# Performance work log

Measured on AMD Instinct MI355X. Metric: run time of the kernel, lower is better.

## Reference

```python
import jax, jax.numpy as jnp
import numpy as np
import math
from jax import lax

B, E, NC, NT, H, W, NH = 16, 256, 8, 8, 64, 64, 8
Q = NC * (NT // 2 + 1)   # 40 prototype tokens
HW = H * W               # in_feature = 4096
OF = 64                  # out_feature; OF*OF == HW required by broadcast


def setup_inputs() -> dict:
    key = jax.random.key(0)
    ks = iter(jax.random.split(key, 48))
    n = lambda s, sc=0.02: jax.random.normal(next(ks), s, jnp.float32) * sc
    return dict(
        query_prototypes=jax.random.normal(next(ks), (B, Q, E), jnp.float32),
        image_embed=jax.random.normal(next(ks), (B, E, H, W), jnp.float32),
        mask_embed=jax.random.normal(next(ks), (B, NC, H, W), jnp.float32),
        masks=jax.random.uniform(next(ks), (B, NC, H, W), jnp.float32),
        ln_g=jnp.ones((E,), jnp.float32), ln_b=jnp.zeros((E,), jnp.float32),
        qw=n((E, E)), qb=jnp.zeros((E,), jnp.float32),
        xp1_w=n((E + NC, E)), xp1_b=jnp.zeros((E,), jnp.float32),
        xp2_w=n((E, E)), xp2_b=jnp.zeros((E,), jnp.float32),
        ln2_g=jnp.ones((E,), jnp.float32), ln2_b=jnp.zeros((E,), jnp.float32),
        dw_w=n((3, 3, 1, E)), dw_b=jnp.zeros((E,), jnp.float32),
        kw=n((E, E)), kb=jnp.zeros((E,), jnp.float32),
        vw=n((E, E)), vb=jnp.zeros((E,), jnp.float32),
        ic_w=n((E,)), ic_b=jnp.zeros((1,), jnp.float32),
        mc_w=n((NC,)), mc_b=jnp.zeros((1,), jnp.float32),
        ipw=n((HW, OF)), ipb=jnp.zeros((OF,), jnp.float32),
        mpw=n((HW, OF)), mpb=jnp.zeros((OF,), jnp.float32),
        cw=n((Q,), 0.1), cb=jnp.zeros((Q,), jnp.float32),
        alpha=jnp.full((HW,), 0.001, jnp.float32),
        beta=jnp.full((HW,), 0.001, jnp.float32),
        ow=n((E, E)), ob=jnp.zeros((E,), jnp.float32),
    )


def _ln(x, g, b, axis):
    m = jnp.mean(x, axis=axis, keepdims=True)
    v = jnp.var(x, axis=axis, keepdims=True)
    return (x - m) * lax.rsqrt(v + 1e-5) * g + b


def reference(query_prototypes, image_embed, mask_embed, masks, ln_g, ln_b, qw, qb,
              xp1_w, xp1_b, xp2_w, xp2_b, ln2_g, ln2_b, dw_w, dw_b, kw, kb, vw, vb,
              ic_w, ic_b, mc_w, mc_b, ipw, ipb, mpw, mpb, cw, cb, alpha, beta, ow, ob):
    hd = E // NH
    # q branch: LayerNorm + Linear
    q = _ln(query_prototypes, ln_g, ln_b, -1) @ qw + qb                      # [B,Q,E]
    # x branch: 1x1 conv + gelu -> 1x1 conv + channel-LN -> depthwise 3x3
    xcat = jnp.concatenate([image_embed, mask_embed], axis=1)                # [B,E+NC,H,W]
    x = jax.nn.gelu(jnp.einsum('bchw,cd->bdhw', xcat, xp1_w) + xp1_b[None, :, None, None], approximate=False)
    x = jnp.einsum('bchw,cd->bdhw', x, xp2_w) + xp2_b[None, :, None, None]
    x = _ln(x, ln2_g[None, :, None, None], ln2_b[None, :, None, None], 1)
    x = lax.conv_general_dilated(x, dw_w, (1, 1), 'SAME',
                                 dimension_numbers=('NCHW', 'HWIO', 'NCHW'),
                                 feature_group_count=E) + dw_b[None, :, None, None]
    x = x.reshape(B, E, HW).transpose(0, 2, 1)                               # [B,HW,E]
    k = (x @ kw + kb).reshape(B, HW, NH, hd).transpose(0, 2, 1, 3)           # [B,NH,HW,hd]
    v = (x @ vw + vb).reshape(B, HW, NH, hd).transpose(0, 2, 1, 3)
    qh = q.reshape(B, Q, NH, hd).transpose(0, 2, 1, 3)                       # [B,NH,Q,hd]
    # class-attention additive bias from rank-1 image x mask outer product
    att_image = (jnp.einsum('behw,e->bhw', image_embed, ic_w) + ic_b[0]).reshape(B, HW) @ ipw + ipb  # [B,OF]
    att_mask = (jnp.einsum('bchw,c->bhw', mask_embed, mc_w) + mc_b[0]).reshape(B, HW) @ mpw + mpb    # [B,OF]
    att_class = att_image[:, :, None] * att_mask[:, None, :]                 # [B,OF,OF]
    att_class = att_class[:, None, :, :] * cw[None, :, None, None] + cb[None, :, None, None]  # 1x1 conv 1->Q
    att_class = att_class.reshape(B, Q, HW)[:, None]                         # [B,1,Q,HW]
    # mask-modulated query-key scores
    att_q = jnp.einsum('bnqc,bnkc->bnqk', qh, k)                             # [B,NH,Q,HW]
    att_q = att_q.reshape(B, NH, NC, NT // 2 + 1, HW) * masks.reshape(B, 1, NC, 1, HW)
    att_q = att_q.reshape(B, NH, Q, HW)
    w = (att_class * alpha + att_q * beta) / math.sqrt(hd)
    w = jax.nn.softmax(w, axis=-1)
    out = jnp.einsum('bnqk,bnkc->bnqc', w, v)                                # [B,NH,Q,hd]
    out = out.transpose(0, 2, 1, 3).reshape(B, Q, E)
    return out @ ow + ob
```

## Files before the change

### kernel.cpp

```cpp
#include <hip/hip_runtime.h>
#include <math.h>

constexpr int B_ = 16, E_ = 256, NC_ = 8, Q_ = 40, H_ = 64, W_ = 64, HW_ = 4096;
constexpr int NH_ = 8, HD_ = 32, OF_ = 64;
constexpr int KP1_ = 320;
constexpr int NPART_ = 32;
constexpr int CH2_ = 32;
constexpr int KVS_ = 512;

typedef __attribute__((ext_vector_type(8))) unsigned short us8;
typedef __attribute__((ext_vector_type(8))) short s8b;
typedef __attribute__((ext_vector_type(4))) short s4b;
typedef __attribute__((ext_vector_type(4))) float f32x4;

__device__ __forceinline__ float gelu_f(float x) {
  return 0.5f * x * (1.0f + erff(x * 0.70710678118654752f));
}
__device__ __forceinline__ float bf2f(unsigned short u) {
  return __uint_as_float(((unsigned int)u) << 16);
}
__device__ __forceinline__ unsigned short f2bf(float f) {
  unsigned int u = __float_as_uint(f);
  u = u + 0x7fff + ((u >> 16) & 1);
  return (unsigned short)(u >> 16);
}
__device__ __forceinline__ unsigned int cvtpk_bf16(float a, float b) {
  unsigned int r;
  asm("v_cvt_pk_bf16_f32 %0, %1, %2" : "=v"(r) : "v"(a), "v"(b));
  return r;
}
__device__ __forceinline__ void gl_lds16(const unsigned short* g, unsigned short* l) {
  __builtin_amdgcn_global_load_lds(
      (const __attribute__((address_space(1))) unsigned int*)g,
      (__attribute__((address_space(3))) unsigned int*)l, 16, 0, 0);
}

__global__ __launch_bounds__(256)
void misc1(const float* __restrict__ w1, const float* __restrict__ w2,
           const float* __restrict__ wk, const float* __restrict__ wv,
           const float* __restrict__ kb, const float* __restrict__ vb,
           unsigned short* __restrict__ o1, unsigned short* __restrict__ o2,
           unsigned short* __restrict__ okv, float* __restrict__ kvbias,
           const float* __restrict__ img, const float* __restrict__ msk,
           unsigned short* __restrict__ xcatT,
           const float* __restrict__ qp, const float* __restrict__ ln_g,
           const float* __restrict__ ln_b, const float* __restrict__ qw,
           const float* __restrict__ qb, float* __restrict__ qbuf,
           const float* __restrict__ icw, const float* __restrict__ icb,
           const float* __restrict__ mcw, const float* __restrict__ mcb,
           float* __restrict__ timg, float* __restrict__ tmsk) {
  __shared__ __align__(16) float smem[64 * 65];
  const int bid = blockIdx.x;
  const int t = threadIdx.x;
  if (bid < 4 * KP1_) {
    const int which = bid / KP1_;
    const int k = bid % KP1_;
    const int n = t;
    if (which == 0) {
      float v = (k < 264) ? w1[(size_t)k * E_ + n] : 0.f;
      o1[(size_t)n * KP1_ + k] = f2bf(v);
    } else if (k < 256) {
      if (which == 1) {
        o2[(size_t)n * 256 + k] = f2bf(w2[(size_t)k * E_ + n]);
      } else if (which == 2) {
        okv[(size_t)n * 256 + k] = f2bf(wk[(size_t)k * E_ + n]);
        if (k == 0) kvbias[n] = kb[n];
      } else {
        okv[(size_t)(256 + n) * 256 + k] = f2bf(wv[(size_t)k * E_ + n]);
        if (k == 0) kvbias[256 + n] = vb[n];
      }
    }
  } else if (bid < 4 * KP1_ + 5120) {
    const int id = bid - 4 * KP1_;
    const int p0 = (id & 63) * 64;
    const int k0 = ((id >> 6) % 5) * 64;
    const int b = id / 320;
    float (*tile)[65] = (float(*)[65])smem;
    const int pg = t & 15;
    const int kg = t >> 4;
    f32x4 v4[4];
    #pragma unroll
    for (int ki = 0; ki < 4; ++ki) {
      const int k = k0 + kg * 4 + ki;
      if (k < 256)
        v4[ki] = *(const f32x4*)(img + ((size_t)b * E_ + k) * HW_ + p0 + pg * 4);
      else if (k < 264)
        v4[ki] = *(const f32x4*)(msk + ((size_t)b * NC_ + (k - 256)) * HW_ + p0 + pg * 4);
      else
        v4[ki] = (f32x4){0.f, 0.f, 0.f, 0.f};
    }
    #pragma unroll
    for (int ki = 0; ki < 4; ++ki)
      #pragma unroll
      for (int j = 0; j < 4; ++j)
        tile[pg * 4 + j][kg * 4 + ki] = v4[ki][j];
    __syncthreads();
    const int pr = t >> 2, ch = t & 3;
    unsigned short st[16];
    #pragma unroll
    for (int i = 0; i < 16; ++i) st[i] = f2bf(tile[pr][ch * 16 + i]);
    unsigned short* dst = xcatT + ((size_t)b * HW_ + p0 + pr) * KP1_ + k0 + ch * 16;
    *(us8*)dst = *(const us8*)&st[0];
    *(us8*)(dst + 8) = *(const us8*)&st[8];
  } else if (bid < 4 * KP1_ + 5120 + 640) {
    const int row = bid - (4 * KP1_ + 5120);
    float* xs = smem;
    float* rs = smem + 272;
    float* rs2 = smem + 280;
    float* sm = smem + 288;
    float x = qp[(size_t)row * E_ + t];
    float s = x, s2 = x * x;
    #pragma unroll
    for (int o = 32; o > 0; o >>= 1) { s += __shfl_down(s, o, 64); s2 += __shfl_down(s2, o, 64); }
    if ((t & 63) == 0) { rs[t >> 6] = s; rs2[t >> 6] = s2; }
    __syncthreads();
    if (t == 0) {
      float S = rs[0] + rs[1] + rs[2] + rs[3];
      float S2 = rs2[0] + rs2[1] + rs2[2] + rs2[3];
      float m = S * (1.0f / E_);
      sm[0] = m;
      sm[1] = rsqrtf(S2 * (1.0f / E_) - m * m + 1e-5f);
    }
    __syncthreads();
    x = (x - sm[0]) * sm[1] * ln_g[t] + ln_b[t];
    xs[t] = x;
    __syncthreads();
    float acc = qb[t];
    #pragma unroll 8
    for (int c = 0; c < E_; ++c) acc += xs[c] * qw[(size_t)c * E_ + t];
    qbuf[(size_t)row * E_ + t] = acc;
  } else {
    const int id = bid - (4 * KP1_ + 5120 + 640);
    const int b = id >> 4;
    const int chunk = id & 15;
    const int lane = t & 63, seg = t >> 6;
    const int p = chunk * 256 + lane * 4;
    f32x4 (*red)[64] = (f32x4(*)[64])smem;
    f32x4 s = (f32x4){0.f, 0.f, 0.f, 0.f};
    const float* ib = img + (size_t)b * E_ * HW_ + p;
    #pragma unroll 8
    for (int e = seg * 64; e < seg * 64 + 64; ++e) {
      const f32x4 v = *(const f32x4*)(ib + (size_t)e * HW_);
      s += v * icw[e];
    }
    red[seg][lane] = s;
    __syncthreads();
    if (seg == 0) {
      f32x4 tot = red[0][lane] + red[1][lane] + red[2][lane] + red[3][lane];
      #pragma unroll
      for (int j = 0; j < 4; ++j) tot[j] += icb[0];
      *(f32x4*)(timg + (size_t)b * HW_ + p) = tot;
      f32x4 s2;
      #pragma unroll
      for (int j = 0; j < 4; ++j) s2[j] = mcb[0];
      const float* mb = msk + (size_t)b * NC_ * HW_ + p;
      #pragma unroll
      for (int c = 0; c < NC_; ++c) {
        const f32x4 mv = *(const f32x4*)(mb + (size_t)c * HW_);
        s2 += mv * mcw[c];
      }
      *(f32x4*)(tmsk + (size_t)b * HW_ + p) = s2;
    }
  }
}

template<int EPI, int KP, int OSTR, int NN>
__global__ __launch_bounds__(256, 4)
void hgemm(const unsigned short* __restrict__ A, const unsigned short* __restrict__ Wt,
           const float* __restrict__ bias, unsigned short* __restrict__ out) {
  constexpr int NT = KP / 64;
  __shared__ __align__(16) unsigned short As[128 * 64];
  __shared__ __align__(16) unsigned short Bs[64 * 64];
  const int t = threadIdx.x;
  const int bid = blockIdx.x;
  const int xcd = bid & 7;
  const int grp = bid >> 3;
  const int m0 = ((grp / NN) * 8 + xcd) * 128;
  const int n0 = (grp % NN) * 64;
  const int w = t >> 6, lane = t & 63;
  const int c = lane & 15, g = lane >> 4;
  const int wm = (w & 1) * 64, wn = (w >> 1) * 32;

  f32x4 acc[4][2];
  #pragma unroll
  for (int i = 0; i < 4; ++i)
    #pragma unroll
    for (int j = 0; j < 2; ++j) acc[i][j] = (f32x4){0.f, 0.f, 0.f, 0.f};

  for (int kt = 0; kt < NT; ++kt) {
    if (kt) __syncthreads();
    #pragma unroll
    for (int i = 0; i < 4; ++i) {
      const int f = i * 256 + t;
      const int row = f >> 3, s = f & 7;
      gl_lds16(A + (size_t)(m0 + row) * KP + kt * 64 + (s ^ (row & 7)) * 8, As + f * 8);
    }
    #pragma unroll
    for (int i = 0; i < 2; ++i) {
      const int f = i * 256 + t;
      const int row = f >> 3, s = f & 7;
      gl_lds16(Wt + (size_t)(n0 + row) * KP + kt * 64 + (s ^ (row & 7)) * 8, Bs + f * 8);
    }
    __syncthreads();
    #pragma unroll
    for (int ks = 0; ks < 2; ++ks) {
      s8b af[4], bf[2];
      #pragma unroll
      for (int mf = 0; mf < 4; ++mf) {
        const int row = wm + mf * 16 + c;
        af[mf] = *(const s8b*)&As[row * 64 + ((ks * 4 + g) ^ (row & 7)) * 8];
      }
      #pragma unroll
      for (int nf = 0; nf < 2; ++nf) {
        const int row = wn + nf * 16 + c;
        bf[nf] = *(const s8b*)&Bs[row * 64 + ((ks * 4 + g) ^ (row & 7)) * 8];
      }
      #pragma unroll
      for (int mf = 0; mf < 4; ++mf)
        #pragma unroll
        for (int nf = 0; nf < 2; ++nf)
          acc[mf][nf] = __builtin_amdgcn_mfma_f32_16x16x32_bf16(af[mf], bf[nf], acc[mf][nf], 0, 0, 0);
    }
  }

  float bv[2];
  #pragma unroll
  for (int nf = 0; nf < 2; ++nf) bv[nf] = bias[n0 + wn + nf * 16 + c];
  __syncthreads();
  #pragma unroll
  for (int mf = 0; mf < 4; ++mf)
    #pragma unroll
    for (int r = 0; r < 4; ++r) {
      const int row = wm + mf * 16 + g * 4 + r;
      #pragma unroll
      for (int nf = 0; nf < 2; ++nf) {
        float v = acc[mf][nf][r] + bv[nf];
        if constexpr (EPI == 0) v = gelu_f(v);
        As[row * 64 + wn + nf * 16 + c] = f2bf(v);
      }
    }
  __syncthreads();
  #pragma unroll
  for (int i = 0; i < 4; ++i) {
    const int f = i * 256 + t;
    const int row = f >> 3, sl = f & 7;
    *(us8*)(out + (size_t)(m0 + row) * OSTR + n0 + sl * 8) = *(const us8*)&As[row * 64 + sl * 8];
  }
}

__global__ __launch_bounds__(256)
void rowstats(const unsigned short* __restrict__ X, float* __restrict__ mean,
              float* __restrict__ rstd) {
  const int row = blockIdx.x * 4 + (threadIdx.x >> 6);
  const int lane = threadIdx.x & 63;
  const uint2 u = *(const uint2*)(X + (size_t)row * E_ + lane * 4);
  float a = bf2f(u.x & 0xffff), b = bf2f(u.x >> 16);
  float c = bf2f(u.y & 0xffff), d = bf2f(u.y >> 16);
  float s = a + b + c + d;
  float s2 = a * a + b * b + c * c + d * d;
  #pragma unroll
  for (int o = 32; o > 0; o >>= 1) { s += __shfl_down(s, o, 64); s2 += __shfl_down(s2, o, 64); }
  if (lane == 0) {
    const float m = s * (1.0f / E_);
    mean[row] = m;
    rstd[row] = rsqrtf(s2 * (1.0f / E_) - m * m + 1e-5f);
  }
}

__global__ __launch_bounds__(256)
void attvec_p(const float* __restrict__ timg, const float* __restrict__ tmsk,
              const float* __restrict__ ipw, const float* __restrict__ mpw,
              float* __restrict__ part) {
  const int chunk = blockIdx.x;
  const int b = blockIdx.y;
  const int mat = blockIdx.z;
  const int o = threadIdx.x & 63, ps = threadIdx.x >> 6;
  const float* tv = (mat ? tmsk : timg) + (size_t)b * HW_ + chunk * 256;
  const float* wp = (mat ? mpw : ipw) + (size_t)chunk * 256 * OF_;
  float s = 0.f;
  #pragma unroll 8
  for (int i = 0; i < 64; ++i) {
    const int p = ps * 64 + i;
    s += tv[p] * wp[(size_t)p * OF_ + o];
  }
  __shared__ float red[4][64];
  red[ps][o] = s;
  __syncthreads();
  if (ps == 0)
    part[(((size_t)b * 2 + mat) * 16 + chunk) * OF_ + o] =
        red[0][o] + red[1][o] + red[2][o] + red[3][o];
}

__global__ __launch_bounds__(256)
void attbias2(const float* __restrict__ part, const float* __restrict__ ipb,
              const float* __restrict__ mpb, const float* __restrict__ alpha,
              const float* __restrict__ beta, float* __restrict__ A1,
              float* __restrict__ asd, float* __restrict__ bsd) {
  __shared__ float aiL[64], amL[64];
  const int b = blockIdx.x;
  const int t = threadIdx.x;
  if (t < 128) {
    const int mat = t >> 6, o = t & 63;
    float v = (mat ? mpb : ipb)[o];
    #pragma unroll
    for (int c = 0; c < 16; ++c)
      v += part[(((size_t)b * 2 + mat) * 16 + c) * OF_ + o];
    if (mat) amL[o] = v; else aiL[o] = v;
  }
  __syncthreads();
  const float scl = 0.17677669529663687f;
  #pragma unroll
  for (int it = 0; it < 16; ++it) {
    const int p = it * 256 + t;
    A1[(size_t)b * HW_ + p] = aiL[p >> 6] * amL[p & 63] * alpha[p] * scl;
    if (b == 0) {
      asd[p] = alpha[p] * scl;
      bsd[p] = beta[p] * scl;
    }
  }
}

__global__ __launch_bounds__(256, 4)
void dwconv_ln4(const unsigned short* __restrict__ X2, const float* __restrict__ mean,
                const float* __restrict__ rstd, const float* __restrict__ g2,
                const float* __restrict__ b2, const float* __restrict__ wgt,
                const float* __restrict__ cbias, unsigned short* __restrict__ out) {
  __shared__ __align__(16) unsigned short xsh[108 * 128];
  __shared__ float msh[108], rsh[108];
  const int t = threadIdx.x;
  const int w0 = blockIdx.x * 16;
  const int h0 = blockIdx.y * 4;
  const int b = blockIdx.z >> 1;
  const int dh = blockIdx.z & 1;
  const int dl = t & 127;
  const int cg = t >> 7;
  const int dgl = dh * 128 + dl;
  const size_t bbase = (size_t)b * HW_;
  for (int f = t; f < 108 * 16; f += 256) {
    const int pix = f >> 4, sl = f & 15;
    const int s = pix / 18, i = pix % 18;
    const int hh = h0 - 1 + s, ww = w0 - 1 + i;
    const bool ok = (hh >= 0 && hh < H_ && ww >= 0 && ww < W_);
    const size_t p = ok ? (bbase + hh * W_ + ww) : bbase;
    gl_lds16(X2 + p * E_ + dh * 128 + sl * 8, &xsh[f * 8]);
  }
  if (t < 108) {
    const int pix = t;
    const int s = pix / 18, i = pix % 18;
    const int hh = h0 - 1 + s, ww = w0 - 1 + i;
    if (hh >= 0 && hh < H_ && ww >= 0 && ww < W_) {
      const size_t p = bbase + hh * W_ + ww;
      msh[pix] = mean[p];
      rsh[pix] = rstd[p];
    } else {
      msh[pix] = 0.f;
      rsh[pix] = 0.f;
    }
  }
  float wq[9];
  #pragma unroll
  for (int i = 0; i < 9; ++i) wq[i] = wgt[i * E_ + dgl];
  const float gg = g2[dgl], bb = b2[dgl], bias = cbias[dgl];
  __syncthreads();
  float o[4][8];
  #pragma unroll
  for (int oy = 0; oy < 4; ++oy)
    #pragma unroll
    for (int j = 0; j < 8; ++j) o[oy][j] = bias;
  #pragma unroll
  for (int s = 0; s < 6; ++s) {
    const int hh = h0 - 1 + s;
    if (hh < 0 || hh >= H_) continue;
    float r[10];
    #pragma unroll
    for (int i = 0; i < 10; ++i) {
      const int rc = cg * 8 + i;
      const int ww = w0 - 1 + rc;
      if (ww >= 0 && ww < W_) {
        const int pix = s * 18 + rc;
        const float x = bf2f(xsh[pix * 128 + dl]);
        r[i] = (x - msh[pix]) * rsh[pix] * gg + bb;
      } else r[i] = 0.f;
    }
    #pragma unroll
    for (int ky = 0; ky < 3; ++ky) {
      const int oy = s - ky;
      if (oy < 0 || oy >= 4) continue;
      const float w_0 = wq[ky * 3], w_1 = wq[ky * 3 + 1], w_2 = wq[ky * 3 + 2];
      #pragma unroll
      for (int j = 0; j < 8; ++j)
        o[oy][j] += r[j] * w_0 + r[j + 1] * w_1 + r[j + 2] * w_2;
    }
  }
  #pragma unroll
  for (int oy = 0; oy < 4; ++oy) {
    const size_t ob_ = bbase + (h0 + oy) * W_ + w0 + cg * 8;
    #pragma unroll
    for (int j = 0; j < 8; ++j) out[(ob_ + j) * E_ + dgl] = f2bf(o[oy][j]);
  }
}

#if __has_builtin(__builtin_amdgcn_mfma_f32_16x16x16bf16_1k)
#define HAVE_MFMA16 1
#else
#define HAVE_MFMA16 0
#endif

__global__ __launch_bounds__(64)
void attn_mfma1w(const float* __restrict__ qbuf, const unsigned short* __restrict__ kv,
                 const float* __restrict__ masks,
                 const float* __restrict__ A1, const float* __restrict__ asd,
                 const float* __restrict__ bsd, const float* __restrict__ cw,
                 const float* __restrict__ cb,
                 float* __restrict__ pacc, float* __restrict__ pm, float* __restrict__ pl) {
  const int bid = blockIdx.x;
  const int xcd = bid & 7;
  const int n = (bid >> 3) & 7;
  const int pb = ((bid >> 6) << 3) | xcd;
  const int ch = pb & 31;
  const int b = pb >> 5;
  const int lane = threadIdx.x;
  const int c = lane & 15, g = lane >> 4;
  __shared__ __align__(16) unsigned short Vt[32 * 72];
#if !HAVE_MFMA16
  __shared__ __align__(16) unsigned short Pl[48 * 72];
#endif

  const size_t bhw = (size_t)b * HW_;
  const int koff = n * HD_;
  const int voff = 256 + koff;
  const int pbase = ch * 128;

  s8b kf2[2][4];
  #pragma unroll
  for (int tile = 0; tile < 2; ++tile) {
    const int p0 = pbase + tile * 64;
    #pragma unroll
    for (int mt = 0; mt < 4; ++mt)
      kf2[tile][mt] = *(const s8b*)(kv + (bhw + p0 + mt * 16 + c) * KVS_ + koff + g * 8);
  }

  s8b qf[3];
  float cwq[3], cbq[3];
  int cls[3];
  #pragma unroll
  for (int nt = 0; nt < 3; ++nt) {
    const int q = nt * 16 + c;
    unsigned short tmp[8];
    if (q < Q_) {
      const float* qp = qbuf + ((size_t)b * Q_ + q) * E_ + koff + g * 8;
      const float4 f0 = *(const float4*)qp;
      const float4 f1 = *(const float4*)(qp + 4);
      tmp[0] = f2bf(f0.x); tmp[1] = f2bf(f0.y); tmp[2] = f2bf(f0.z); tmp[3] = f2bf(f0.w);
      tmp[4] = f2bf(f1.x); tmp[5] = f2bf(f1.y); tmp[6] = f2bf(f1.z); tmp[7] = f2bf(f1.w);
      cwq[nt] = cw[q]; cbq[nt] = cb[q];
    } else {
      #pragma unroll
      for (int i = 0; i < 8; ++i) tmp[i] = 0;
      cwq[nt] = 0.f; cbq[nt] = 0.f;
    }
    qf[nt] = *(const s8b*)tmp;
    cls[nt] = min(q / 5, NC_ - 1);
  }

  f32x4 acc_oT[3][2];
  #pragma unroll
  for (int qt = 0; qt < 3; ++qt)
    #pragma unroll
    for (int dt = 0; dt < 2; ++dt) acc_oT[qt][dt] = (f32x4){0.f, 0.f, 0.f, 0.f};
  float m_r[3] = {-1e30f, -1e30f, -1e30f};
  float l_r[3] = {0.f, 0.f, 0.f};
  float scv[3] = {1.f, 1.f, 1.f};

  #pragma unroll
  for (int tile = 0; tile < 2; ++tile) {
    const int p0 = pbase + tile * 64;
    us8 vr[4];
    #pragma unroll
    for (int cp = 0; cp < 4; ++cp)
      vr[cp] = *(const us8*)(kv + (bhw + p0 + lane) * KVS_ + voff + cp * 8);
    f32x4 sa[3][4];
    __builtin_amdgcn_s_setprio(1);
    #pragma unroll
    for (int nt = 0; nt < 3; ++nt)
      #pragma unroll
      for (int mt = 0; mt < 4; ++mt)
        sa[nt][mt] = __builtin_amdgcn_mfma_f32_16x16x32_bf16(kf2[tile][mt], qf[nt],
                     (f32x4){0.f, 0.f, 0.f, 0.f}, 0, 0, 0);
    __builtin_amdgcn_s_setprio(0);
    #pragma unroll
    for (int cp = 0; cp < 4; ++cp) {
      #pragma unroll
      for (int i = 0; i < 8; ++i) Vt[(cp * 8 + i) * 72 + lane] = vr[cp][i];
    }
    f32x4 A1v[4], asv[4], bsv[4];
    #pragma unroll
    for (int mt = 0; mt < 4; ++mt) {
      const int pp = p0 + mt * 16 + g * 4;
      A1v[mt] = *(const f32x4*)(A1 + bhw + pp);
      asv[mt] = *(const f32x4*)(asd + pp);
      bsv[mt] = *(const f32x4*)(bsd + pp);
    }
    uint2 pwv[3][4];
    #pragma unroll
    for (int nt = 0; nt < 3; ++nt) {
      const float* mrow = masks + ((size_t)b * NC_ + cls[nt]) * HW_;
      f32x4 att[4];
      #pragma unroll
      for (int mt = 0; mt < 4; ++mt) {
        const f32x4 mk = *(const f32x4*)(mrow + p0 + mt * 16 + g * 4);
        att[mt] = A1v[mt] * cwq[nt] + asv[mt] * cbq[nt] + sa[nt][mt] * mk * bsv[mt];
      }
      float mx = -1e30f;
      #pragma unroll
      for (int mt = 0; mt < 4; ++mt)
        mx = fmaxf(mx, fmaxf(fmaxf(att[mt][0], att[mt][1]), fmaxf(att[mt][2], att[mt][3])));
      mx = fmaxf(mx, __shfl_xor(mx, 16));
      mx = fmaxf(mx, __shfl_xor(mx, 32));
      const float newm = fmaxf(m_r[nt], mx);
      const float sc = __expf(m_r[nt] - newm);
      m_r[nt] = newm;
      scv[nt] = sc;
      float sum = 0.f;
      #pragma unroll
      for (int mt = 0; mt < 4; ++mt) {
        #pragma unroll
        for (int i = 0; i < 4; ++i) att[mt][i] = __expf(att[mt][i] - newm);
        sum += (att[mt][0] + att[mt][1]) + (att[mt][2] + att[mt][3]);
        pwv[nt][mt].x = cvtpk_bf16(att[mt][0], att[mt][1]);
        pwv[nt][mt].y = cvtpk_bf16(att[mt][2], att[mt][3]);
      }
      sum += __shfl_xor(sum, 16);
      sum += __shfl_xor(sum, 32);
      l_r[nt] = l_r[nt] * sc + sum;
    }
    #pragma unroll
    for (int nt = 0; nt < 3; ++nt)
      #pragma unroll
      for (int dt = 0; dt < 2; ++dt)
        #pragma unroll
        for (int r = 0; r < 4; ++r) acc_oT[nt][dt][r] *= scv[nt];
#if HAVE_MFMA16
    __builtin_amdgcn_s_setprio(1);
    #pragma unroll
    for (int mt = 0; mt < 4; ++mt) {
      s4b vf[2];
      #pragma unroll
      for (int dt = 0; dt < 2; ++dt)
        vf[dt] = *(const s4b*)&Vt[(dt * 16 + c) * 72 + mt * 16 + g * 4];
      #pragma unroll
      for (int nt = 0; nt < 3; ++nt)
        #pragma unroll
        for (int dt = 0; dt < 2; ++dt)
          acc_oT[nt][dt] = __builtin_amdgcn_mfma_f32_16x16x16bf16_1k(
              vf[dt], *(const s4b*)&pwv[nt][mt], acc_oT[nt][dt], 0, 0, 0);
    }
    __builtin_amdgcn_s_setprio(0);
#else
    #pragma unroll
    for (int nt = 0; nt < 3; ++nt)
      #pragma unroll
      for (int mt = 0; mt < 4; ++mt)
        *(uint2*)&Pl[(nt * 16 + c) * 72 + mt * 16 + g * 4] = pwv[nt][mt];
    #pragma unroll
    for (int ks = 0; ks < 2; ++ks) {
      s8b pf[3], vf2[2];
      #pragma unroll
      for (int nt = 0; nt < 3; ++nt)
        pf[nt] = *(const s8b*)&Pl[(nt * 16 + c) * 72 + ks * 32 + g * 8];
      #pragma unroll
      for (int dt = 0; dt < 2; ++dt)
        vf2[dt] = *(const s8b*)&Vt[(dt * 16 + c) * 72 + ks * 32 + g * 8];
      #pragma unroll
      for (int nt = 0; nt < 3; ++nt)
        #pragma unroll
        for (int dt = 0; dt < 2; ++dt)
          acc_oT[nt][dt] = __builtin_amdgcn_mfma_f32_16x16x32_bf16(vf2[dt], pf[nt], acc_oT[nt][dt], 0, 0, 0);
    }
#endif
  }
  const int pidx = ((b * NH_ + n) * NPART_) + ch;
  #pragma unroll
  for (int nt = 0; nt < 3; ++nt) {
    const int q = nt * 16 + c;
    if (q < Q_) {
      #pragma unroll
      for (int dt = 0; dt < 2; ++dt)
        *(f32x4*)&pacc[((size_t)pidx * Q_ + q) * HD_ + dt * 16 + g * 4] = acc_oT[nt][dt];
    }
  }
  if (g == 0) {
    #pragma unroll
    for (int nt = 0; nt < 3; ++nt) {
      const int q = nt * 16 + c;
      if (q < Q_) {
        pm[(size_t)pidx * Q_ + q] = m_r[nt];
        pl[(size_t)pidx * Q_ + q] = l_r[nt];
      }
    }
  }
}

__global__ __launch_bounds__(256)
void cfinal(const float* __restrict__ pacc, const float* __restrict__ pm,
            const float* __restrict__ pl, const float* __restrict__ ow,
            const float* __restrict__ ob, float* __restrict__ out) {
  __shared__ float xs[E_];
  const int row = blockIdx.x;
  const int q = row % Q_;
  const int b = row / Q_;
  const int e = threadIdx.x;
  const int n = e >> 5, d = e & 31;
  const int base = (b * NH_ + n) * NPART_;
  float M = -1e30f;
  #pragma unroll
  for (int cc = 0; cc < NPART_; ++cc) M = fmaxf(M, pm[(size_t)(base + cc) * Q_ + q]);
  float L = 0.f, O = 0.f;
  #pragma unroll
  for (int cc = 0; cc < NPART_; ++cc) {
    const size_t o2 = (size_t)(base + cc) * Q_ + q;
    const float w = __expf(pm[o2] - M);
    L += pl[o2] * w;
    O += pacc[o2 * HD_ + d] * w;
  }
  xs[e] = O / L;
  __syncthreads();
  float acc = ob[e];
  #pragma unroll 8
  for (int c = 0; c < E_; ++c) acc += xs[c] * ow[(size_t)c * E_ + e];
  out[(size_t)row * E_ + e] = acc;
}

extern "C" void kernel_launch(void* const* d_in, const int* in_sizes, int n_in,
                              void* d_out, int out_size, void* d_ws, size_t ws_size,
                              hipStream_t stream) {
  (void)in_sizes; (void)n_in; (void)out_size; (void)ws_size;
  const float* qp    = (const float*)d_in[0];
  const float* img   = (const float*)d_in[1];
  const float* msk   = (const float*)d_in[2];
  const float* masks = (const float*)d_in[3];
  const float* ln_g  = (const float*)d_in[4];
  const float* ln_b  = (const float*)d_in[5];
  const float* qw    = (const float*)d_in[6];
  const float* qb    = (const float*)d_in[7];
  const float* x1w   = (const float*)d_in[8];
  const float* x1b   = (const float*)d_in[9];
  const float* x2w   = (const float*)d_in[10];
  const float* x2b   = (const float*)d_in[11];
  const float* ln2g  = (const float*)d_in[12];
  const float* ln2b  = (const float*)d_in[13];
  const float* dww   = (const float*)d_in[14];
  const float* dwb   = (const float*)d_in[15];
  const float* kw    = (const float*)d_in[16];
  const float* kb    = (const float*)d_in[17];
  const float* vw    = (const float*)d_in[18];
  const float* vb    = (const float*)d_in[19];
  const float* icw   = (const float*)d_in[20];
  const float* icb   = (const float*)d_in[21];
  const float* mcw   = (const float*)d_in[22];
  const float* mcb   = (const float*)d_in[23];
  const float* ipw   = (const float*)d_in[24];
  const float* ipb   = (const float*)d_in[25];
  const float* mpw   = (const float*)d_in[26];
  const float* mpb   = (const float*)d_in[27];
  const float* cw    = (const float*)d_in[28];
  const float* cb    = (const float*)d_in[29];
  const float* alpha = (const float*)d_in[30];
  const float* beta  = (const float*)d_in[31];
  const float* ow    = (const float*)d_in[32];
  const float* ob    = (const float*)d_in[33];

  char* wsb = (char*)d_ws;
  const size_t MB = 1024 * 1024;
  unsigned short* xcatT = (unsigned short*)(wsb);
  unsigned short* xf    = xcatT;
  unsigned short* x1buf = (unsigned short*)(wsb + 42 * MB);
  unsigned short* x2    = (unsigned short*)(wsb + 76 * MB);
  unsigned short* kv    = (unsigned short*)(wsb + 76 * MB);
  unsigned short* wt1 = (unsigned short*)(wsb + 141 * MB);
  unsigned short* wt2 = wt1 + 256 * KP1_;
  unsigned short* wtkv = wt2 + 256 * 256;
  float* fb    = (float*)(wsb + 143 * MB);
  float* kvbias = fb;
  float* qbuf  = kvbias + 512;
  float* meanb = qbuf + (size_t)B_ * Q_ * E_;
  float* rstdb = meanb + (size_t)B_ * HW_;
  float* timg  = rstdb + (size_t)B_ * HW_;
  float* tmsk  = timg + (size_t)B_ * HW_;
  float* A1b   = tmsk + (size_t)B_ * HW_;
  float* asdb  = A1b + (size_t)B_ * HW_;
  float* bsdb  = asdb + HW_;
  float* pacc  = bsdb + HW_;
  float* pmb   = pacc + (size_t)B_ * NH_ * NPART_ * Q_ * HD_;
  float* plb   = pmb + (size_t)B_ * NH_ * NPART_ * Q_;
  float* partv = plb + (size_t)B_ * NH_ * NPART_ * Q_;

  misc1<<<dim3(4 * KP1_ + 5120 + 640 + 256), dim3(256), 0, stream>>>(
      x1w, x2w, kw, vw, kb, vb, wt1, wt2, wtkv, kvbias,
      img, msk, xcatT, qp, ln_g, ln_b, qw, qb, qbuf,
      icw, icb, mcw, mcb, timg, tmsk);
  attvec_p<<<dim3(16, B_, 2), dim3(256), 0, stream>>>(timg, tmsk, ipw, mpw, partv);
  attbias2<<<dim3(B_), dim3(256), 0, stream>>>(partv, ipb, mpb, alpha, beta, A1b, asdb, bsdb);
  hgemm<0, KP1_, 256, 4><<<dim3(512 * 4), dim3(256), 0, stream>>>(xcatT, wt1, x1b, x1buf);
  hgemm<1, 256, 256, 4><<<dim3(512 * 4), dim3(256), 0, stream>>>(x1buf, wt2, x2b, x2);
  rowstats<<<dim3(B_ * HW_ / 4), dim3(256), 0, stream>>>(x2, meanb, rstdb);
  dwconv_ln4<<<dim3(4, 16, B_ * 2), dim3(256), 0, stream>>>(x2, meanb, rstdb, ln2g, ln2b, dww, dwb, xf);
  hgemm<1, 256, KVS_, 8><<<dim3(512 * 8), dim3(256), 0, stream>>>(xf, wtkv, kvbias, kv);
  attn_mfma1w<<<dim3(CH2_ * NH_ * B_), dim3(64), 0, stream>>>(qbuf, kv, masks, A1b, asdb, bsdb,
                                                              cw, cb, pacc, pmb, plb);
  cfinal<<<dim3(B_ * Q_), dim3(256), 0, stream>>>(pacc, pmb, plb, ow, ob, (float*)d_out);
}
```

Baseline: 202.1 us.

## Fuse input transpose and bf16 conversion into first GEMM's A-tile load

Removes the separate transpose pass that wrote a bf16 pixel-major copy of image and mask embeddings, and instead has a new GEMM kernel load fp32 activations directly, convert with packed bf16 instructions and store swizzled into LDS. This eliminates a large intermediate write and re-read. The trade-off is that each N-tile block re-reads the fp32 input, doing more global traffic per tile and conversion work inside the GEMM loop, without the async global-to-LDS path for A.

```diff
diff --git a/kernel.cpp b/kernel.cpp
--- a/kernel.cpp
+++ b/kernel.cpp
@@ -42,7 +42,6 @@
            unsigned short* __restrict__ o1, unsigned short* __restrict__ o2,
            unsigned short* __restrict__ okv, float* __restrict__ kvbias,
            const float* __restrict__ img, const float* __restrict__ msk,
-           unsigned short* __restrict__ xcatT,
            const float* __restrict__ qp, const float* __restrict__ ln_g,
            const float* __restrict__ ln_b, const float* __restrict__ qw,
            const float* __restrict__ qb, float* __restrict__ qbuf,
@@ -70,40 +69,8 @@
         if (k == 0) kvbias[256 + n] = vb[n];
       }
     }
-  } else if (bid < 4 * KP1_ + 5120) {
-    const int id = bid - 4 * KP1_;
-    const int p0 = (id & 63) * 64;
-    const int k0 = ((id >> 6) % 5) * 64;
-    const int b = id / 320;
-    float (*tile)[65] = (float(*)[65])smem;
-    const int pg = t & 15;
-    const int kg = t >> 4;
-    f32x4 v4[4];
-    #pragma unroll
-    for (int ki = 0; ki < 4; ++ki) {
-      const int k = k0 + kg * 4 + ki;
-      if (k < 256)
-        v4[ki] = *(const f32x4*)(img + ((size_t)b * E_ + k) * HW_ + p0 + pg * 4);
-      else if (k < 264)
-        v4[ki] = *(const f32x4*)(msk + ((size_t)b * NC_ + (k - 256)) * HW_ + p0 + pg * 4);
-      else
-        v4[ki] = (f32x4){0.f, 0.f, 0.f, 0.f};
-    }
-    #pragma unroll
-    for (int ki = 0; ki < 4; ++ki)
-      #pragma unroll
-      for (int j = 0; j < 4; ++j)
-        tile[pg * 4 + j][kg * 4 + ki] = v4[ki][j];
-    __syncthreads();
-    const int pr = t >> 2, ch = t & 3;
-    unsigned short st[16];
-    #pragma unroll
-    for (int i = 0; i < 16; ++i) st[i] = f2bf(tile[pr][ch * 16 + i]);
-    unsigned short* dst = xcatT + ((size_t)b * HW_ + p0 + pr) * KP1_ + k0 + ch * 16;
-    *(us8*)dst = *(const us8*)&st[0];
-    *(us8*)(dst + 8) = *(const us8*)&st[8];
-  } else if (bid < 4 * KP1_ + 5120 + 640) {
-    const int row = bid - (4 * KP1_ + 5120);
+  } else if (bid < 4 * KP1_ + 640) {
+    const int row = bid - 4 * KP1_;
     float* xs = smem;
     float* rs = smem + 272;
     float* rs2 = smem + 280;
@@ -130,7 +97,7 @@
     for (int c = 0; c < E_; ++c) acc += xs[c] * qw[(size_t)c * E_ + t];
     qbuf[(size_t)row * E_ + t] = acc;
   } else {
-    const int id = bid - (4 * KP1_ + 5120 + 640);
+    const int id = bid - (4 * KP1_ + 640);
     const int b = id >> 4;
     const int chunk = id & 15;
     const int lane = t & 63, seg = t >> 6;
@@ -245,6 +212,110 @@
     const int f = i * 256 + t;
     const int row = f >> 3, sl = f & 7;
     *(us8*)(out + (size_t)(m0 + row) * OSTR + n0 + sl * 8) = *(const us8*)&As[row * 64 + sl * 8];
+  }
+}
+
+__global__ __launch_bounds__(256, 4)
+void hgemm1f(const float* __restrict__ img, const float* __restrict__ msk,
+             const unsigned short* __restrict__ Wt,
+             const float* __restrict__ bias, unsigned short* __restrict__ out) {
+  constexpr int KP = KP1_;
+  constexpr int NT = 5;
+  constexpr int NN = 4;
+  __shared__ __align__(16) unsigned short As[128 * 64];
+  __shared__ __align__(16) unsigned short Bs[64 * 64];
+  const int t = threadIdx.x;
+  const int bid = blockIdx.x;
+  const int xcd = bid & 7;
+  const int grp = bid >> 3;
+  const int m0 = ((grp / NN) * 8 + xcd) * 128;
+  const int n0 = (grp % NN) * 64;
+  const int b = m0 >> 12;
+  const int px0 = m0 & 4095;
+  const int w = t >> 6, lane = t & 63;
+  const int c = lane & 15, g = lane >> 4;
+  const int wm = (w & 1) * 64, wn = (w >> 1) * 32;
+  const int pg = t & 31;
+  const int kg = t >> 5;
+
+  f32x4 acc[4][2];
+  #pragma unroll
+  for (int i = 0; i < 4; ++i)
+    #pragma unroll
+    for (int j = 0; j < 2; ++j) acc[i][j] = (f32x4){0.f, 0.f, 0.f, 0.f};
+
+  for (int kt = 0; kt < NT; ++kt) {
+    if (kt) __syncthreads();
+    #pragma unroll
+    for (int i = 0; i < 2; ++i) {
+      const int f = i * 256 + t;
+      const int row = f >> 3, s = f & 7;
+      gl_lds16(Wt + (size_t)(n0 + row) * KP + kt * 64 + (s ^ (row & 7)) * 8, Bs + f * 8);
+    }
+    f32x4 ar[8];
+    #pragma unroll
+    for (int i = 0; i < 8; ++i) {
+      const int k = kt * 64 + kg * 8 + i;
+      if (k < 256)
+        ar[i] = *(const f32x4*)(img + ((size_t)b * E_ + k) * HW_ + px0 + pg * 4);
+      else if (k < 264)
+        ar[i] = *(const f32x4*)(msk + ((size_t)b * NC_ + (k - 256)) * HW_ + px0 + pg * 4);
+      else
+        ar[i] = (f32x4){0.f, 0.f, 0.f, 0.f};
+    }
+    #pragma unroll
+    for (int j = 0; j < 4; ++j) {
+      const int px = pg * 4 + j;
+      uint4 pk;
+      pk.x = cvtpk_bf16(ar[0][j], ar[1][j]);
+      pk.y = cvtpk_bf16(ar[2][j], ar[3][j]);
+      pk.z = cvtpk_bf16(ar[4][j], ar[5][j]);
+      pk.w = cvtpk_bf16(ar[6][j], ar[7][j]);
+      *(uint4*)&As[px * 64 + (kg ^ (px & 7)) * 8] = pk;
+    }
+    __syncthreads();
+    #pragma unroll
+    for (int ks = 0; ks < 2; ++ks) {
+      s8b af[4], bf[2];
+      #pragma unroll
+      for (int mf = 0; mf < 4; ++mf) {
+        const int row = wm + mf * 16 + c;
+        af[mf] = *(const s8b*)&As[row * 64 + ((ks * 4 + g) ^ (row & 7)) * 8];
+      }
+      #pragma unroll
+      for (int nf = 0; nf < 2; ++nf) {
+        const int row = wn + nf * 16 + c;
+        bf[nf] = *(const s8b*)&Bs[row * 64 + ((ks * 4 + g) ^ (row & 7)) * 8];
+      }
+      #pragma unroll
+      for (int mf = 0; mf < 4; ++mf)
+        #pragma unroll
+        for (int nf = 0; nf < 2; ++nf)
+          acc[mf][nf] = __builtin_amdgcn_mfma_f32_16x16x32_bf16(af[mf], bf[nf], acc[mf][nf], 0, 0, 0);
+    }
+  }
+
+  float bv[2];
+  #pragma unroll
+  for (int nf = 0; nf < 2; ++nf) bv[nf] = bias[n0 + wn + nf * 16 + c];
+  __syncthreads();
+  #pragma unroll
+  for (int mf = 0; mf < 4; ++mf)
+    #pragma unroll
+    for (int r = 0; r < 4; ++r) {
+      const int row = wm + mf * 16 + g * 4 + r;
+      #pragma unroll
+      for (int nf = 0; nf < 2; ++nf) {
+        float v = gelu_f(acc[mf][nf][r] + bv[nf]);
+        As[row * 64 + wn + nf * 16 + c] = f2bf(v);
+      }
+    }
+  __syncthreads();
+  #pragma unroll
+  for (int i = 0; i < 4; ++i) {
+    const int f = i * 256 + t;
+    const int row = f >> 3, sl = f & 7;
+    *(us8*)(out + (size_t)(m0 + row) * 256 + n0 + sl * 8) = *(const us8*)&As[row * 64 + sl * 8];
   }
 }
 
@@ -672,8 +743,7 @@
 
   char* wsb = (char*)d_ws;
   const size_t MB = 1024 * 1024;
-  unsigned short* xcatT = (unsigned short*)(wsb);
-  unsigned short* xf    = xcatT;
+  unsigned short* xf    = (unsigned short*)(wsb);
   unsigned short* x1buf = (unsigned short*)(wsb + 42 * MB);
   unsigned short* x2    = (unsigned short*)(wsb + 76 * MB);
   unsigned short* kv    = (unsigned short*)(wsb + 76 * MB);
@@ -695,13 +765,13 @@
   float* plb   = pmb + (size_t)B_ * NH_ * NPART_ * Q_;
   float* partv = plb + (size_t)B_ * NH_ * NPART_ * Q_;
 
-  misc1<<<dim3(4 * KP1_ + 5120 + 640 + 256), dim3(256), 0, stream>>>(
+  misc1<<<dim3(4 * KP1_ + 640 + 256), dim3(256), 0, stream>>>(
       x1w, x2w, kw, vw, kb, vb, wt1, wt2, wtkv, kvbias,
-      img, msk, xcatT, qp, ln_g, ln_b, qw, qb, qbuf,
+      img, msk, qp, ln_g, ln_b, qw, qb, qbuf,
       icw, icb, mcw, mcb, timg, tmsk);
   attvec_p<<<dim3(16, B_, 2), dim3(256), 0, stream>>>(timg, tmsk, ipw, mpw, partv);
   attbias2<<<dim3(B_), dim3(256), 0, stream>>>(partv, ipb, mpb, alpha, beta, A1b, asdb, bsdb);
-  hgemm<0, KP1_, 256, 4><<<dim3(512 * 4), dim3(256), 0, stream>>>(xcatT, wt1, x1b, x1buf);
+  hgemm1f<<<dim3(512 * 4), dim3(256), 0, stream>>>(img, msk, wt1, x1b, x1buf);
   hgemm<1, 256, 256, 4><<<dim3(512 * 4), dim3(256), 0, stream>>>(x1buf, wt2, x2b, x2);
   rowstats<<<dim3(B_ * HW_ / 4), dim3(256), 0, stream>>>(x2, meanb, rstdb);
   dwconv_ln4<<<dim3(4, 16, B_ * 2), dim3(256), 0, stream>>>(x2, meanb, rstdb, ln2g, ln2b, dww, dwb, xf);
```

After: 198.7 us. Within noise of the previous version (-1.7%).
